# Kernel optimization log

Measured on AMD Instinct MI355X. Metric: run time of the kernel, lower is better.

Reference implementation:

```python
import jax, jax.numpy as jnp
import numpy as np

B, N, D, K = 2048, 65536, 256, 32
TEMP = 0.1  # config.temperature
EPS = 1e-4  # constant from -log(1 - sim + 0.0001)


def setup_inputs() -> dict:
    key = jax.random.key(0)
    k1, k2, k3, k4 = jax.random.split(key, 4)
    x = jax.random.normal(k1, (B, D), jnp.float32)
    x = x / jnp.linalg.norm(x, axis=-1, keepdims=True)  # unit-sphere latents
    mu = jax.random.normal(k2, (N, D), jnp.float32)
    mu = mu / jnp.linalg.norm(mu, axis=-1, keepdims=True)  # splat centers on sphere
    alpha = jax.random.uniform(k3, (N,), jnp.float32, 0.5, 2.0)  # splat sharpness > 0
    W = jax.random.normal(k4, (1, 3), jnp.float32) * 0.5  # W_comp: Linear(3,1)
    b = jnp.zeros((1,), jnp.float32)
    return {"x": x, "mu": mu, "alpha": alpha, "W": W, "b": b, "knn_k": K}


def reference(x, mu, alpha, W, b, knn_k):
    # --- kNN over splat store by dot-product similarity ---
    sims = x @ mu.T                               # [B, N]
    vals, idx = jax.lax.top_k(sims, knn_k)        # [B, K]; vals == bmm(neighbors_mu, x)

    # --- E_splats(x) = -logsumexp(alpha_k * (x.mu_k - 1) / tau) ---
    a = alpha[idx]                                # [B, K] gathered neighbor alphas
    exponent = a * (vals - 1.0) / TEMP
    e_splat = -jax.nn.logsumexp(exponent, axis=-1)  # [B]

    # --- E_geom: mean over off-diagonal pairs of -log(1 - x_i.x_j + eps) ---
    bs = x @ x.T                                  # [B, B]
    Bn = x.shape[0]
    offdiag = ~jnp.eye(Bn, dtype=bool)
    terms = -jnp.log(1.0 - bs + EPS)
    e_geom = jnp.sum(jnp.where(offdiag, terms, 0.0)) / (Bn * (Bn - 1))

    # --- E_comp: sigmoid(W.[u, v, u*v] + b) with u, v = top-2 neighbor dots ---
    u = vals[:, 0:1]                              # [B, 1]
    v = vals[:, 1:2]                              # [B, 1]
    uv = jnp.concatenate([u, v, u * v], axis=-1)  # [B, 3]
    e_comp = jax.nn.sigmoid(uv @ W.T + b)[:, 0]   # [B]

    return e_splat + 0.01 * e_geom + 0.05 * e_comp
```

## Files before the change

kernel.cpp:

```cpp
#include <hip/hip_runtime.h>
#include <hip/hip_bf16.h>
#include <math.h>

#define BDIM 2048
#define NDIM 65536
#define DDIM 256
#define KTOP 32
#define TEMP_INV 10.0f
#define EPS_GEOM 1e-4f

#define TSEL  0.18f
#define TSEL8 0.17f
#define CAP 512
#define KPL (CAP / 64)

#define SCRN_BLOCKS ((BDIM / 128) * (NDIM / 128))
#define EG_BLOCKS   ((BDIM / 128) * (BDIM / 128))
#define XP_BLOCKS   (BDIM * DDIM / 2048)
#define MP_BLOCKS   (NDIM * DDIM / 2048)
#define MUF_BLOCKS  (NDIM / 16)
#define XF_BLOCKS   (BDIM / 16)

typedef unsigned long long u64;
typedef __attribute__((ext_vector_type(8))) short bf16x8;
typedef __attribute__((ext_vector_type(4))) float f32x4;

#define GLD16(gptr, lptr)                                                     \
  __builtin_amdgcn_global_load_lds(                                           \
      (const __attribute__((address_space(1))) void*)(gptr),                  \
      (__attribute__((address_space(3))) void*)(lptr), 16, 0, 0)

__device__ __forceinline__ float bflo(unsigned u) { return __uint_as_float(u << 16); }
__device__ __forceinline__ float bfhi(unsigned u) { return __uint_as_float(u & 0xffff0000u); }

__device__ __forceinline__ float loadInput(const void* p, int i, int isf32) {
  if (isf32) return ((const float*)p)[i];
  return __uint_as_float(((unsigned)((const unsigned short*)p)[i]) << 16);
}

__device__ __forceinline__ short f2bf(float f) {
  const unsigned u = __float_as_uint(f);
  return (short)((u + 0x7fffu + ((u >> 16) & 1u)) >> 16);
}

__device__ __forceinline__ void load8f(const void* p, size_t i, int isf32, float* f) {
  if (isf32) {
    const float* gp = (const float*)p + i;
    const float4 a = *(const float4*)gp;
    const float4 b = *(const float4*)(gp + 4);
    f[0] = a.x; f[1] = a.y; f[2] = a.z; f[3] = a.w;
    f[4] = b.x; f[5] = b.y; f[6] = b.z; f[7] = b.w;
  } else {
    const uint4 q = *(const uint4*)((const unsigned short*)p + i);
    f[0] = bflo(q.x); f[1] = bfhi(q.x); f[2] = bflo(q.y); f[3] = bfhi(q.y);
    f[4] = bflo(q.z); f[5] = bfhi(q.z); f[6] = bflo(q.w); f[7] = bfhi(q.w);
  }
}

__device__ __forceinline__ uint2 pk8fp8(const float* f) {
  int w0 = 0, w1 = 0;
  w0 = __builtin_amdgcn_cvt_pk_fp8_f32(f[0], f[1], w0, false);
  w0 = __builtin_amdgcn_cvt_pk_fp8_f32(f[2], f[3], w0, true);
  w1 = __builtin_amdgcn_cvt_pk_fp8_f32(f[4], f[5], w1, false);
  w1 = __builtin_amdgcn_cvt_pk_fp8_f32(f[6], f[7], w1, true);
  uint2 r; r.x = (unsigned)w0; r.y = (unsigned)w1; return r;
}

__device__ __forceinline__ long long mk64(unsigned lo, unsigned hi) {
  return (long long)(((u64)hi << 32) | (u64)lo);
}

__device__ __forceinline__ unsigned enc32(float f) {
  const unsigned u = __float_as_uint(f);
  return u ^ ((u & 0x80000000u) ? 0xFFFFFFFFu : 0x80000000u);
}
__device__ __forceinline__ float dec32(unsigned c) {
  const unsigned u = (c & 0x80000000u) ? (c ^ 0x80000000u) : ~c;
  return __uint_as_float(u);
}

__global__ __launch_bounds__(256)
void detect_init_kernel(const void* __restrict__ x, const void* __restrict__ mu,
                        const void* __restrict__ alpha, const void* __restrict__ W,
                        int* __restrict__ flags, float* __restrict__ egeom,
                        int* __restrict__ cnt) {
  const int tid = threadIdx.x;
  for (int i = tid; i < BDIM; i += 256) cnt[i] = 0;
  if (tid == 0) *egeom = 0.f;

  const int t = tid >> 6, lane = tid & 63;
  const void* ptrs[4] = { x, mu, alpha, W };
  const int   nel[4]  = { BDIM * DDIM, NDIM * DDIM, NDIM, 3 };
  const unsigned* p = (const unsigned*)ptrs[t];
  int nw = nel[t] / 2;
  if (nw > 2048) nw = 2048;
  int sane = 0, tot = 0;
  for (int i = lane; i < nw; i += 64) {
    const unsigned lo = p[i] & 0xffffu;
    const int eb = (int)((lo >> 7) & 0xffu);
    sane += (lo == 0u || (eb >= 96 && eb <= 160)) ? 1 : 0;
    tot  += 1;
  }
  #pragma unroll
  for (int off = 1; off < 64; off <<= 1) {
    sane += __shfl_xor(sane, off);
    tot  += __shfl_xor(tot, off);
  }
  if (lane == 0) flags[t] = (2 * sane < tot) ? 1 : 0;
}

__global__ __launch_bounds__(256)
void prep_kernel(const void* __restrict__ x, const void* __restrict__ mu,
                 const int* __restrict__ flags,
                 unsigned short* __restrict__ xb, unsigned short* __restrict__ mub,
                 unsigned char* __restrict__ x8f, unsigned char* __restrict__ mu8f,
                 const int use_fp8, const int use_mub) {
  const int bx = blockIdx.x;
  const int tid = threadIdx.x;
  if (bx < XP_BLOCKS) {
    const size_t i = ((size_t)bx * 256 + tid) * 8;
    float f[8];
    load8f(x, i, flags[0], f);
    bf16x8 v;
    #pragma unroll
    for (int j = 0; j < 8; ++j) v[j] = f2bf(f[j]);
    *(bf16x8*)(xb + i) = v;
    return;
  }
  if (use_fp8) {
    __shared__ float sm[16][257];
    const bool isx = (bx >= XP_BLOCKS + MUF_BLOCKS);
    const int rg = isx ? (bx - XP_BLOCKS - MUF_BLOCKS) : (bx - XP_BLOCKS);
    const void* src = isx ? x : mu;
    const int isf32 = isx ? flags[0] : flags[1];
    unsigned char* dst = (isx ? x8f : mu8f) + (size_t)rg * 4096;
    #pragma unroll
    for (int j = 0; j < 16; ++j)
      sm[j][tid] = loadInput(src, (rg * 16 + j) * DDIM + tid, isf32);
    __syncthreads();
    const int p = tid >> 6, L = tid & 63;
    const int r = L & 15, c0 = p * 64 + ((L >> 4) & 3) * 8;
    float f0[8], f1[8];
    #pragma unroll
    for (int j = 0; j < 8; ++j) { f0[j] = sm[r][c0 + j]; f1[j] = sm[r][c0 + 32 + j]; }
    const uint2 lo = pk8fp8(f0), hi = pk8fp8(f1);
    uint4 o; o.x = lo.x; o.y = lo.y; o.z = hi.x; o.w = hi.y;
    *(uint4*)(dst + (size_t)p * 1024 + (size_t)L * 16) = o;
  } else {
    if (!use_mub || !flags[1]) return;
    const size_t i = (((size_t)(bx - XP_BLOCKS)) * 256 + tid) * 8;
    float f[8];
    load8f(mu, i, 1, f);
    bf16x8 v;
    #pragma unroll
    for (int j = 0; j < 8; ++j) v[j] = f2bf(f[j]);
    *(bf16x8*)(mub + i) = v;
  }
}

__global__ __launch_bounds__(256, 3)
void gemm_fp8_kernel(const unsigned char* __restrict__ x8f,
                     const unsigned char* __restrict__ mu8f,
                     int* __restrict__ cnt, int* __restrict__ cidx,
                     float* __restrict__ accum) {
  __shared__ float red[4];
  const int tid = threadIdx.x;
  const int w = tid >> 6, L = tid & 63;
  const int rw = w >> 1, cw = w & 1;
  const int midx = L & 15;

  const int h = blockIdx.x;
  const bool is_eg = (h >= SCRN_BLOCKS);
  int row0, col0;
  const unsigned char* bsrc;
  if (is_eg) {
    const int eb = h - SCRN_BLOCKS;
    row0 = (eb >> 4) * 128;
    col0 = (eb & 15) * 128;
    bsrc = x8f;
  } else {
    const int lid = (h & 7) * 1024 + (h >> 3);
    row0 = (lid & 15) * 128;
    col0 = (lid >> 4) * 128;
    bsrc = mu8f;
  }

  const unsigned char* ab = x8f + ((size_t)((row0 >> 4) + rw * 4)) * 4096 + (size_t)L * 16;
  const unsigned char* bb = bsrc + ((size_t)((col0 >> 4) + cw * 4)) * 4096 + (size_t)L * 16;

  f32x4 acc[4][4];
  #pragma unroll
  for (int g = 0; g < 4; ++g)
    #pragma unroll
    for (int c = 0; c < 4; ++c)
      acc[g][c] = (f32x4){0.f, 0.f, 0.f, 0.f};

  #pragma unroll
  for (int p = 0; p < 4; ++p) {
    uint4 av[4], bv[4];
    #pragma unroll
    for (int g = 0; g < 4; ++g)
      av[g] = *(const uint4*)(ab + (size_t)g * 4096 + (size_t)p * 1024);
    #pragma unroll
    for (int c = 0; c < 4; ++c)
      bv[c] = *(const uint4*)(bb + (size_t)c * 4096 + (size_t)p * 1024);
    #pragma unroll
    for (int g = 0; g < 4; ++g)
      #pragma unroll
      for (int c = 0; c < 4; ++c) {
        acc[g][c] = __builtin_amdgcn_mfma_f32_16x16x32_fp8_fp8(
            mk64(av[g].x, av[g].y), mk64(bv[c].x, bv[c].y), acc[g][c], 0, 0, 0);
        acc[g][c] = __builtin_amdgcn_mfma_f32_16x16x32_fp8_fp8(
            mk64(av[g].z, av[g].w), mk64(bv[c].z, bv[c].w), acc[g][c], 0, 0, 0);
      }
  }

  const int quad4 = (L >> 4) * 4;
  if (!is_eg) {
    #pragma unroll
    for (int g = 0; g < 4; ++g) {
      const int rowb = row0 + rw * 64 + g * 16 + quad4;
      #pragma unroll
      for (int c = 0; c < 4; ++c) {
        const int col = col0 + cw * 64 + c * 16 + midx;
        #pragma unroll
        for (int t = 0; t < 4; ++t) {
          if (acc[g][c][t] >= TSEL8) {
            const int row = rowb + t;
            const int pos = atomicAdd(&cnt[row], 1);
            if (pos < CAP) cidx[row * CAP + pos] = col;
          }
        }
      }
    }
  } else {
    float local = 0.f;
    #pragma unroll
    for (int g = 0; g < 4; ++g) {
      const int rowb = row0 + rw * 64 + g * 16 + quad4;
      #pragma unroll
      for (int c = 0; c < 4; ++c) {
        const int col = col0 + cw * 64 + c * 16 + midx;
        #pragma unroll
        for (int t = 0; t < 4; ++t) {
          if (rowb + t != col) {
            float arg = 1.0f - acc[g][c][t] + EPS_GEOM;
            arg = fmaxf(arg, 1e-20f);
            local += -logf(arg);
          }
        }
      }
    }
    #pragma unroll
    for (int off = 1; off < 64; off <<= 1) local += __shfl_xor(local, off);
    if (L == 0) red[w] = local;
    __syncthreads();
    if (tid == 0) atomicAdd(accum, red[0] + red[1] + red[2] + red[3]);
  }
}

__global__ __launch_bounds__(256, 3)
void gemm_bf16_kernel(const unsigned short* __restrict__ xb, const void* __restrict__ mu,
                      const unsigned short* __restrict__ mub, const int use_mub,
                      const int* __restrict__ flags,
                      int* __restrict__ cnt, int* __restrict__ cidx,
                      float* __restrict__ accum) {
  __shared__ __align__(16) unsigned char As[2][8 * 1024];
  __shared__ __align__(16) unsigned char Bs[2][8 * 1024];
  __shared__ float red[4];
  const int tid = threadIdx.x;
  const int w = tid >> 6, L = tid & 63;
  const int midx = L & 15;
  const int koff = (L >> 4) * 8;
  const int rw = w >> 1, cw = w & 1;

  const int h = blockIdx.x;
  const bool is_eg = (h >= SCRN_BLOCKS);
  int row0, col0, bfast;
  const unsigned short* bs16;
  if (is_eg) {
    const int eb = h - SCRN_BLOCKS;
    col0 = (eb & 15) * 128;
    row0 = (eb >> 4) * 128;
    bs16 = xb;
    bfast = 1;
  } else {
    const int lid = (h & 7) * 1024 + (h >> 3);
    row0 = (lid & 15) * 128;
    col0 = (lid >> 4) * 128;
    const int isf32m = flags[1];
    bs16 = isf32m ? mub : (const unsigned short*)mu;
    bfast = (!isf32m) || use_mub;
  }

  f32x4 acc[4][4];
  #pragma unroll
  for (int g = 0; g < 4; ++g)
    #pragma unroll
    for (int c = 0; c < 4; ++c)
      acc[g][c] = (f32x4){0.f, 0.f, 0.f, 0.f};

  auto stage = [&](int kc, int buf) {
    #pragma unroll
    for (int q = 0; q < 4; ++q) {
      const int t = w * 4 + q;
      if (t < 8) {
        const size_t ge = (size_t)(row0 + t * 16 + midx) * DDIM + kc + koff;
        GLD16(xb + ge, As[buf] + (size_t)t * 1024);
      } else {
        const int hb = t - 8;
        const size_t ge = (size_t)(col0 + hb * 16 + midx) * DDIM + kc + koff;
        if (bfast) {
          GLD16(bs16 + ge, Bs[buf] + (size_t)hb * 1024);
        } else {
          const float* gp = (const float*)mu + ge;
          const float4 f0 = *(const float4*)gp;
          const float4 f1 = *(const float4*)(gp + 4);
          bf16x8 v;
          v[0] = f2bf(f0.x); v[1] = f2bf(f0.y); v[2] = f2bf(f0.z); v[3] = f2bf(f0.w);
          v[4] = f2bf(f1.x); v[5] = f2bf(f1.y); v[6] = f2bf(f1.z); v[7] = f2bf(f1.w);
          *((bf16x8*)(Bs[buf] + (size_t)hb * 1024 + (size_t)L * 16)) = v;
        }
      }
    }
  };

  stage(0, 0);
  __syncthreads();
  int cur = 0;
  for (int kc = 32; kc <= DDIM; kc += 32) {
    if (kc < DDIM) stage(kc, cur ^ 1);
    bf16x8 af[4], bfr[4];
    #pragma unroll
    for (int g = 0; g < 4; ++g)
      af[g] = *(const bf16x8*)(As[cur] + (size_t)(rw * 4 + g) * 1024 + (size_t)L * 16);
    #pragma unroll
    for (int c = 0; c < 4; ++c)
      bfr[c] = *(const bf16x8*)(Bs[cur] + (size_t)(cw * 4 + c) * 1024 + (size_t)L * 16);
    #pragma unroll
    for (int g = 0; g < 4; ++g)
      #pragma unroll
      for (int c = 0; c < 4; ++c)
        acc[g][c] = __builtin_amdgcn_mfma_f32_16x16x32_bf16(af[g], bfr[c], acc[g][c], 0, 0, 0);
    __syncthreads();
    cur ^= 1;
  }

  const int quad4 = (L >> 4) * 4;
  if (!is_eg) {
    #pragma unroll
    for (int g = 0; g < 4; ++g) {
      const int rowb = row0 + rw * 64 + g * 16 + quad4;
      #pragma unroll
      for (int c = 0; c < 4; ++c) {
        const int col = col0 + cw * 64 + c * 16 + midx;
        #pragma unroll
        for (int t = 0; t < 4; ++t) {
          if (acc[g][c][t] >= TSEL) {
            const int row = rowb + t;
            const int pos = atomicAdd(&cnt[row], 1);
            if (pos < CAP) cidx[row * CAP + pos] = col;
          }
        }
      }
    }
  } else {
    float local = 0.f;
    #pragma unroll
    for (int g = 0; g < 4; ++g) {
      const int rowb = row0 + rw * 64 + g * 16 + quad4;
      #pragma unroll
      for (int c = 0; c < 4; ++c) {
        const int col = col0 + cw * 64 + c * 16 + midx;
        #pragma unroll
        for (int t = 0; t < 4; ++t) {
          if (rowb + t != col) {
            float arg = 1.0f - acc[g][c][t] + EPS_GEOM;
            arg = fmaxf(arg, 1e-20f);
            local += -logf(arg);
          }
        }
      }
    }
    #pragma unroll
    for (int off = 1; off < 64; off <<= 1) local += __shfl_xor(local, off);
    if (L == 0) red[w] = local;
    __syncthreads();
    if (tid == 0) atomicAdd(accum, red[0] + red[1] + red[2] + red[3]);
  }
}

__global__ __launch_bounds__(256)
void final_kernel(const int* __restrict__ cnt, const int* __restrict__ cidx,
                  const void* __restrict__ x, const void* __restrict__ mu,
                  const void* __restrict__ alpha, const void* __restrict__ W,
                  const void* __restrict__ bptr, const float* __restrict__ egeom,
                  const int* __restrict__ flags, float* __restrict__ out) {
  __shared__ float xrow[DDIM];
  __shared__ float cv[CAP];
  __shared__ float tv[KTOP];
  __shared__ int   tix[KTOP];
  const int tid = threadIdx.x;
  const int w = tid >> 6, L = tid & 63;
  const int half = L >> 5, hl = L & 31;
  const int row = blockIdx.x;
  const int isf32x = flags[0], isf32m = flags[1];
  const int isf32a = flags[2], isf32w = flags[3];
  int n = cnt[row]; if (n > CAP) n = CAP;

  for (int i = tid; i < DDIM; i += 256)
    xrow[i] = loadInput(x, row * DDIM + i, isf32x);
  __syncthreads();

  float x8r[8];
  #pragma unroll
  for (int j = 0; j < 8; ++j) x8r[j] = xrow[hl * 8 + j];

  for (int base = w * 2; base < n; base += 8) {
    const int cno = base + half;
    float s = 0.f;
    if (cno < n) {
      const int col = cidx[row * CAP + cno];
      const size_t e = (size_t)col * DDIM + hl * 8;
      float m8[8];
      if (isf32m) {
        const float* gp = (const float*)mu + e;
        const float4 f0 = *(const float4*)gp;
        const float4 f1 = *(const float4*)(gp + 4);
        m8[0] = f0.x; m8[1] = f0.y; m8[2] = f0.z; m8[3] = f0.w;
        m8[4] = f1.x; m8[5] = f1.y; m8[6] = f1.z; m8[7] = f1.w;
      } else {
        const uint4 q = *(const uint4*)((const unsigned short*)mu + e);
        m8[0] = bflo(q.x); m8[1] = bfhi(q.x); m8[2] = bflo(q.y); m8[3] = bfhi(q.y);
        m8[4] = bflo(q.z); m8[5] = bfhi(q.z); m8[6] = bflo(q.w); m8[7] = bfhi(q.w);
      }
      #pragma unroll
      for (int j = 0; j < 8; ++j) s += x8r[j] * m8[j];
    }
    #pragma unroll
    for (int off = 1; off < 32; off <<= 1) s += __shfl_xor(s, off);
    if (hl == 0 && cno < n) cv[cno] = s;
  }
  __syncthreads();
  if (tid >= 64) return;

  u64 key[KPL];
  #pragma unroll
  for (int j = 0; j < KPL; ++j) {
    const int sidx = j * 64 + L;
    key[j] = 0;
    if (sidx < n)
      key[j] = ((u64)enc32(cv[sidx]) << 32) |
               (u64)(0xFFFFFFFFu - (unsigned)cidx[row * CAP + sidx]);
  }
  for (int round = 0; round < KTOP; ++round) {
    u64 lm = key[0];
    #pragma unroll
    for (int j = 1; j < KPL; ++j) lm = (key[j] > lm) ? key[j] : lm;
    u64 wm = lm;
    #pragma unroll
    for (int off = 1; off < 64; off <<= 1) {
      const unsigned lo = __shfl_xor((unsigned)wm, off);
      const unsigned hi = __shfl_xor((unsigned)(wm >> 32), off);
      const u64 o = ((u64)hi << 32) | lo;
      wm = (o > wm) ? o : wm;
    }
    #pragma unroll
    for (int j = 0; j < KPL; ++j) if (key[j] == wm) key[j] = 0;
    if (L == 0) {
      if (wm != 0) {
        tv[round]  = dec32((unsigned)(wm >> 32));
        tix[round] = (int)(0xFFFFFFFFu - (unsigned)(wm & 0xFFFFFFFFu));
      } else { tv[round] = 0.f; tix[round] = 0; }
    }
  }

  float e = -1e30f;
  if (L < KTOP) {
    const float a = loadInput(alpha, tix[L], isf32a);
    e = a * (tv[L] - 1.0f) * TEMP_INV;
  }
  float m = e;
  #pragma unroll
  for (int off = 1; off < 64; off <<= 1) m = fmaxf(m, __shfl_xor(m, off));
  float p = (L < KTOP) ? expf(e - m) : 0.f;
  #pragma unroll
  for (int off = 1; off < 64; off <<= 1) p += __shfl_xor(p, off);

  if (L == 0) {
    const float e_splat = -(m + logf(p));
    const float uu = tv[0], vv = tv[1];
    const float W0 = loadInput(W, 0, isf32w), W1 = loadInput(W, 1, isf32w);
    const float W2 = loadInput(W, 2, isf32w), b0 = loadInput(bptr, 0, isf32w);
    const float z = W0 * uu + W1 * vv + W2 * uu * vv + b0;
    const float e_comp = 1.0f / (1.0f + expf(-z));
    const float eg = egeom[0] * (1.0f / ((float)BDIM * (float)(BDIM - 1)));
    out[row] = e_splat + 0.01f * eg + 0.05f * e_comp;
  }
}

extern "C" void kernel_launch(void* const* d_in, const int* in_sizes, int n_in,
                              void* d_out, int out_size, void* d_ws, size_t ws_size,
                              hipStream_t stream) {
  const void* x     = d_in[0];
  const void* mu    = d_in[1];
  const void* alpha = d_in[2];
  const void* W     = d_in[3];
  const void* b     = d_in[4];

  char* ws = (char*)d_ws;
  int*            flags = (int*)ws;
  float*          egeom = (float*)(ws + 64);
  int*            cnt   = (int*)(ws + 256);
  int*            cidx  = (int*)(ws + 8448);
  unsigned short* xb    = (unsigned short*)(ws + 8448 + (size_t)BDIM * CAP * 4);
  const size_t    AUX_OFF = 8448 + (size_t)BDIM * CAP * 4 + (size_t)BDIM * DDIM * 2;
  const size_t    X8_BYTES  = (size_t)BDIM * DDIM;
  const size_t    MU8_BYTES = (size_t)NDIM * DDIM;
  const int       use_fp8 = (ws_size >= AUX_OFF + X8_BYTES + MU8_BYTES) ? 1 : 0;
  unsigned char*  x8f   = (unsigned char*)(ws + AUX_OFF);
  unsigned char*  mu8f  = (unsigned char*)(ws + AUX_OFF + X8_BYTES);
  const size_t    MUB_BYTES = (size_t)NDIM * DDIM * 2;
  const int       use_mub = (!use_fp8 && ws_size >= AUX_OFF + MUB_BYTES) ? 1 : 0;
  unsigned short* mub   = (unsigned short*)(ws + (use_mub ? AUX_OFF : 0));
  float*          out   = (float*)d_out;

  detect_init_kernel<<<1, 256, 0, stream>>>(x, mu, alpha, W, flags, egeom, cnt);
  const int nprep = XP_BLOCKS + (use_fp8 ? (MUF_BLOCKS + XF_BLOCKS)
                                         : (use_mub ? MP_BLOCKS : 0));
  prep_kernel<<<nprep, 256, 0, stream>>>(
      x, mu, flags, xb, mub, x8f, mu8f, use_fp8, use_mub);
  if (use_fp8) {
    gemm_fp8_kernel<<<SCRN_BLOCKS + EG_BLOCKS, 256, 0, stream>>>(
        x8f, mu8f, cnt, cidx, egeom);
  } else {
    gemm_bf16_kernel<<<SCRN_BLOCKS + EG_BLOCKS, 256, 0, stream>>>(
        xb, mu, mub, use_mub, flags, cnt, cidx, egeom);
  }
  final_kernel<<<BDIM, 256, 0, stream>>>(cnt, cidx, x, mu, alpha, W, b, egeom, flags, out);
}
```

Before: 314.1 us.

## Pack screen scores with candidates and refine only the top-64 exactly

The screening pass now stores a bf16 approximation of each candidate's similarity alongside its column index. The final kernel uses a bitwise radix search on these packed scores to keep only about 64 candidates per row before the exact fp32 dot products, instead of all of them. The fp8 MFMA loop double-buffers its register loads, and the fp8 pack stage loads with vector reads. Packing the column into 16 bits only works because N is 65536, and pruning by approximate fp8 scores risks dropping true top-32 neighbours if screening errors exceed the margin.

```diff
diff --git a/kernel.cpp b/kernel.cpp
--- a/kernel.cpp
+++ b/kernel.cpp
@@ -13,6 +13,7 @@
 #define TSEL8 0.17f
 #define CAP 512
 #define KPL (CAP / 64)
+#define REFINE 64
 
 #define SCRN_BLOCKS ((BDIM / 128) * (NDIM / 128))
 #define EG_BLOCKS   ((BDIM / 128) * (BDIM / 128))
@@ -68,6 +69,10 @@
 
 __device__ __forceinline__ long long mk64(unsigned lo, unsigned hi) {
   return (long long)(((u64)hi << 32) | (u64)lo);
+}
+
+__device__ __forceinline__ unsigned packCand(float sim, int col) {
+  return (((unsigned)(unsigned short)f2bf(sim)) << 16) | (0xFFFFu - (unsigned)col);
 }
 
 __device__ __forceinline__ unsigned enc32(float f) {
@@ -134,9 +139,26 @@
     const void* src = isx ? x : mu;
     const int isf32 = isx ? flags[0] : flags[1];
     unsigned char* dst = (isx ? x8f : mu8f) + (size_t)rg * 4096;
-    #pragma unroll
-    for (int j = 0; j < 16; ++j)
-      sm[j][tid] = loadInput(src, (rg * 16 + j) * DDIM + tid, isf32);
+    if (isf32) {
+      const float* s32 = (const float*)src + (size_t)rg * 16 * DDIM;
+      #pragma unroll
+      for (int q = 0; q < 4; ++q) {
+        const int idx = q * 256 + tid;
+        const int r = idx >> 6, c4 = (idx & 63) * 4;
+        const float4 v = *(const float4*)(s32 + (size_t)r * DDIM + c4);
+        sm[r][c4] = v.x; sm[r][c4 + 1] = v.y; sm[r][c4 + 2] = v.z; sm[r][c4 + 3] = v.w;
+      }
+    } else {
+      #pragma unroll
+      for (int q = 0; q < 2; ++q) {
+        const int idx = q * 256 + tid;
+        const int r = idx >> 5, c8 = (idx & 31) * 8;
+        float f[8];
+        load8f(src, (size_t)(rg * 16 + r) * DDIM + c8, 0, f);
+        #pragma unroll
+        for (int j = 0; j < 8; ++j) sm[r][c8 + j] = f[j];
+      }
+    }
     __syncthreads();
     const int p = tid >> 6, L = tid & 63;
     const int r = L & 15, c0 = p * 64 + ((L >> 4) & 3) * 8;
@@ -195,23 +217,31 @@
     for (int c = 0; c < 4; ++c)
       acc[g][c] = (f32x4){0.f, 0.f, 0.f, 0.f};
 
+  uint4 av[2][4], bv[2][4];
+  #pragma unroll
+  for (int g = 0; g < 4; ++g) av[0][g] = *(const uint4*)(ab + (size_t)g * 4096);
+  #pragma unroll
+  for (int c = 0; c < 4; ++c) bv[0][c] = *(const uint4*)(bb + (size_t)c * 4096);
+
   #pragma unroll
   for (int p = 0; p < 4; ++p) {
-    uint4 av[4], bv[4];
-    #pragma unroll
-    for (int g = 0; g < 4; ++g)
-      av[g] = *(const uint4*)(ab + (size_t)g * 4096 + (size_t)p * 1024);
-    #pragma unroll
-    for (int c = 0; c < 4; ++c)
-      bv[c] = *(const uint4*)(bb + (size_t)c * 4096 + (size_t)p * 1024);
+    const int cb = p & 1, nb = cb ^ 1;
+    if (p < 3) {
+      #pragma unroll
+      for (int g = 0; g < 4; ++g)
+        av[nb][g] = *(const uint4*)(ab + (size_t)g * 4096 + (size_t)(p + 1) * 1024);
+      #pragma unroll
+      for (int c = 0; c < 4; ++c)
+        bv[nb][c] = *(const uint4*)(bb + (size_t)c * 4096 + (size_t)(p + 1) * 1024);
+    }
     #pragma unroll
     for (int g = 0; g < 4; ++g)
       #pragma unroll
       for (int c = 0; c < 4; ++c) {
         acc[g][c] = __builtin_amdgcn_mfma_f32_16x16x32_fp8_fp8(
-            mk64(av[g].x, av[g].y), mk64(bv[c].x, bv[c].y), acc[g][c], 0, 0, 0);
+            mk64(av[cb][g].x, av[cb][g].y), mk64(bv[cb][c].x, bv[cb][c].y), acc[g][c], 0, 0, 0);
         acc[g][c] = __builtin_amdgcn_mfma_f32_16x16x32_fp8_fp8(
-            mk64(av[g].z, av[g].w), mk64(bv[c].z, bv[c].w), acc[g][c], 0, 0, 0);
+            mk64(av[cb][g].z, av[cb][g].w), mk64(bv[cb][c].z, bv[cb][c].w), acc[g][c], 0, 0, 0);
       }
   }
 
@@ -228,7 +258,7 @@
           if (acc[g][c][t] >= TSEL8) {
             const int row = rowb + t;
             const int pos = atomicAdd(&cnt[row], 1);
-            if (pos < CAP) cidx[row * CAP + pos] = col;
+            if (pos < CAP) cidx[row * CAP + pos] = (int)packCand(acc[g][c][t], col);
           }
         }
       }
@@ -359,7 +389,7 @@
           if (acc[g][c][t] >= TSEL) {
             const int row = rowb + t;
             const int pos = atomicAdd(&cnt[row], 1);
-            if (pos < CAP) cidx[row * CAP + pos] = col;
+            if (pos < CAP) cidx[row * CAP + pos] = (int)packCand(acc[g][c][t], col);
           }
         }
       }
@@ -397,9 +427,11 @@
                   const void* __restrict__ bptr, const float* __restrict__ egeom,
                   const int* __restrict__ flags, float* __restrict__ out) {
   __shared__ float xrow[DDIM];
+  __shared__ int   scol[CAP];
   __shared__ float cv[CAP];
   __shared__ float tv[KTOP];
   __shared__ int   tix[KTOP];
+  __shared__ int   selcnt;
   const int tid = threadIdx.x;
   const int w = tid >> 6, L = tid & 63;
   const int half = L >> 5, hl = L & 31;
@@ -407,20 +439,52 @@
   const int isf32x = flags[0], isf32m = flags[1];
   const int isf32a = flags[2], isf32w = flags[3];
   int n = cnt[row]; if (n > CAP) n = CAP;
+  if (tid == 0) selcnt = 0;
 
   for (int i = tid; i < DDIM; i += 256)
     xrow[i] = loadInput(x, row * DDIM + i, isf32x);
   __syncthreads();
 
+  if (w == 0) {
+    unsigned ent[KPL], v16[KPL];
+    #pragma unroll
+    for (int j = 0; j < KPL; ++j) {
+      const int sidx = j * 64 + L;
+      ent[j] = (sidx < n) ? (unsigned)cidx[row * CAP + sidx] : 0u;
+      v16[j] = ent[j] >> 16;
+    }
+    unsigned T = 0;
+    if (n > REFINE) {
+      for (int bit = 15; bit >= 0; --bit) {
+        const unsigned candT = T | (1u << bit);
+        int c = 0;
+        #pragma unroll
+        for (int j = 0; j < KPL; ++j) c += (v16[j] >= candT) ? 1 : 0;
+        #pragma unroll
+        for (int off = 1; off < 64; off <<= 1) c += __shfl_xor(c, off);
+        if (c >= REFINE) T = candT;
+      }
+    }
+    #pragma unroll
+    for (int j = 0; j < KPL; ++j) {
+      if (ent[j] != 0u && v16[j] >= T) {
+        const int p = atomicAdd(&selcnt, 1);
+        scol[p] = (int)(0xFFFFu - (ent[j] & 0xFFFFu));
+      }
+    }
+  }
+  __syncthreads();
+  const int m = selcnt;
+
   float x8r[8];
   #pragma unroll
   for (int j = 0; j < 8; ++j) x8r[j] = xrow[hl * 8 + j];
 
-  for (int base = w * 2; base < n; base += 8) {
+  for (int base = w * 2; base < m; base += 8) {
     const int cno = base + half;
     float s = 0.f;
-    if (cno < n) {
-      const int col = cidx[row * CAP + cno];
+    if (cno < m) {
+      const int col = scol[cno];
       const size_t e = (size_t)col * DDIM + hl * 8;
       float m8[8];
       if (isf32m) {
@@ -439,7 +503,7 @@
     }
     #pragma unroll
     for (int off = 1; off < 32; off <<= 1) s += __shfl_xor(s, off);
-    if (hl == 0 && cno < n) cv[cno] = s;
+    if (hl == 0 && cno < m) cv[cno] = s;
   }
   __syncthreads();
   if (tid >= 64) return;
@@ -449,9 +513,9 @@
   for (int j = 0; j < KPL; ++j) {
     const int sidx = j * 64 + L;
     key[j] = 0;
-    if (sidx < n)
+    if (sidx < m)
       key[j] = ((u64)enc32(cv[sidx]) << 32) |
-               (u64)(0xFFFFFFFFu - (unsigned)cidx[row * CAP + sidx]);
+               (u64)(0xFFFFFFFFu - (unsigned)scol[sidx]);
   }
   for (int round = 0; round < KTOP; ++round) {
     u64 lm = key[0];
@@ -480,15 +544,15 @@
     const float a = loadInput(alpha, tix[L], isf32a);
     e = a * (tv[L] - 1.0f) * TEMP_INV;
   }
-  float m = e;
-  #pragma unroll
-  for (int off = 1; off < 64; off <<= 1) m = fmaxf(m, __shfl_xor(m, off));
-  float p = (L < KTOP) ? expf(e - m) : 0.f;
+  float mx = e;
+  #pragma unroll
+  for (int off = 1; off < 64; off <<= 1) mx = fmaxf(mx, __shfl_xor(mx, off));
+  float p = (L < KTOP) ? expf(e - mx) : 0.f;
   #pragma unroll
   for (int off = 1; off < 64; off <<= 1) p += __shfl_xor(p, off);
 
   if (L == 0) {
-    const float e_splat = -(m + logf(p));
+    const float e_splat = -(mx + logf(p));
     const float uu = tv[0], vv = tv[1];
     const float W0 = loadInput(W, 0, isf32w), W1 = loadInput(W, 1, isf32w);
     const float W2 = loadInput(W, 2, isf32w), b0 = loadInput(bptr, 0, isf32w);
```

New measurement: 302.2 us. 3.8% less time.
